# Performance work log

Hardware: AMD Instinct MI355X
Metric: run time of the kernel (lower is better)

## Reference

```python
import jax, jax.numpy as jnp
import numpy as np

B, L, H, E = 8, 4096, 8, 64
NEIGH = 128          # neigh_size: local window length (entries per row of band mask)
SPLITS = 32          # number of Q blocks
L1 = L // SPLITS     # rows per block = 128 (neigh_size <= L/splits holds with equality)


def setup_inputs() -> dict:
    key = jax.random.key(0)
    kq, kk, kv = jax.random.split(key, 3)
    return {
        "queries": jax.random.normal(kq, (B, L, H, E), jnp.float32),
        "keys":    jax.random.normal(kk, (B, L, H, E), jnp.float32),
        "values":  jax.random.normal(kv, (B, L, H, E), jnp.float32),
    }


def reference(queries, keys, values):
    scale = 1.0 / np.sqrt(E)
    # Global key index of each entry in a KV block: block j covers [j*l1 - neigh, j*l1 + l1)
    kv_idx = (jnp.arange(SPLITS)[:, None] * L1
              + jnp.arange(L1 + NEIGH)[None, :] - NEIGH)      # [splits, l1+neigh]
    kv_gather = jnp.clip(kv_idx, 0, L - 1)                    # out-of-range entries get masked

    Qb = queries.reshape(B, SPLITS, L1, H, E)                 # [B, j, l, H, E]
    Kb = keys[:, kv_gather]                                   # [B, j, m, H, E]
    Vb = values[:, kv_gather]                                 # [B, j, m, H, E]

    scores = jnp.einsum('bjlhe,bjmhe->bhjlm', Qb, Kb) * scale # [B, H, splits, l1, l1+neigh]

    # Band: key global index k satisfies q - neigh < k <= q  <=>  l < m <= l + neigh
    l_idx = jnp.arange(L1)[:, None]
    m_idx = jnp.arange(L1 + NEIGH)[None, :]
    band = (m_idx > l_idx) & (m_idx <= l_idx + NEIGH)         # [l1, l1+neigh]
    valid = band[None, :, :] & (kv_idx[:, None, :] >= 0)      # [splits, l1, l1+neigh]

    scores = jnp.where(valid[None, None], scores, jnp.float32(-1e9))
    attn = jax.nn.softmax(scores, axis=-1)
    out = jnp.einsum('bhjlm,bjmhe->bjlhe', attn, Vb)          # [B, splits, l1, H, E]
    return out.reshape(B, L, H, E)
```

## Files before the change

kernel.cpp:

```cpp
#include <hip/hip_runtime.h>

#define B_ 8
#define L_ 4096
#define H_ 8
#define E_ 64
#define NEIGH_ 128
#define SPLITS_ 32
#define BQ 128
#define WIN 256
#define QPAD 72
#define VPAD 264

typedef float f32x4 __attribute__((ext_vector_type(4)));
typedef __bf16 bf16x8 __attribute__((ext_vector_type(8)));
typedef unsigned short u16x4 __attribute__((ext_vector_type(4)));
typedef unsigned short u16x8 __attribute__((ext_vector_type(8)));

__device__ inline unsigned short f2bf(float f) {
  unsigned int u = __float_as_uint(f);
  u += 0x7fff + ((u >> 16) & 1);
  return (unsigned short)(u >> 16);
}

__global__ __launch_bounds__(512) void la_kernel(
    const float* __restrict__ Q, const float* __restrict__ K,
    const float* __restrict__ V, float* __restrict__ out) {
  const int j = blockIdx.x, h = blockIdx.y, b = blockIdx.z;
  const int t = threadIdx.x;

  __shared__ unsigned short Qs[BQ * QPAD];
  __shared__ unsigned short Ks[WIN * QPAD];
  __shared__ unsigned short VsT[E_ * VPAD];
  __shared__ unsigned short Ps[BQ * VPAD];

  const int q0 = j * BQ;
  const int g0 = q0 - NEIGH_;

  for (int i = 0; i < 4; ++i) {
    int idx = t + i * 512;
    int row = idx >> 4, c4 = idx & 15;
    const float4 v = *(const float4*)(Q + ((((size_t)b * L_) + q0 + row) * H_ + h) * E_ + c4 * 4);
    u16x4 p = { f2bf(v.x), f2bf(v.y), f2bf(v.z), f2bf(v.w) };
    *(u16x4*)&Qs[row * QPAD + c4 * 4] = p;
  }
  for (int i = 0; i < 8; ++i) {
    int idx = t + i * 512;
    int km = idx >> 4, c4 = idx & 15;
    int g = g0 + km; g = g < 0 ? 0 : g;
    const float4 v = *(const float4*)(K + ((((size_t)b * L_) + g) * H_ + h) * E_ + c4 * 4);
    u16x4 p = { f2bf(v.x), f2bf(v.y), f2bf(v.z), f2bf(v.w) };
    *(u16x4*)&Ks[km * QPAD + c4 * 4] = p;
  }
  for (int i = 0; i < 8; ++i) {
    int idx = t + i * 512;
    int km = idx >> 4, c4 = idx & 15;
    int g = g0 + km; g = g < 0 ? 0 : g;
    const float4 v = *(const float4*)(V + ((((size_t)b * L_) + g) * H_ + h) * E_ + c4 * 4);
    VsT[(c4 * 4 + 0) * VPAD + km] = f2bf(v.x);
    VsT[(c4 * 4 + 1) * VPAD + km] = f2bf(v.y);
    VsT[(c4 * 4 + 2) * VPAD + km] = f2bf(v.z);
    VsT[(c4 * 4 + 3) * VPAD + km] = f2bf(v.w);
  }
  __syncthreads();

  const int wv = t >> 6, lane = t & 63;
  const int l15 = lane & 15, quad = lane >> 4;
  const int r0 = wv * 16;

  f32x4 S[16];
  for (int kt = 0; kt < 16; ++kt) S[kt] = (f32x4){0.f, 0.f, 0.f, 0.f};
  for (int ks = 0; ks < 2; ++ks) {
    bf16x8 a = __builtin_bit_cast(bf16x8,
        *(const u16x8*)&Qs[(r0 + l15) * QPAD + ks * 32 + quad * 8]);
    for (int kt = 0; kt < 16; ++kt) {
      bf16x8 bb = __builtin_bit_cast(bf16x8,
          *(const u16x8*)&Ks[(kt * 16 + l15) * QPAD + ks * 32 + quad * 8]);
      S[kt] = __builtin_amdgcn_mfma_f32_16x16x32_bf16(a, bb, S[kt], 0, 0, 0);
    }
  }

  float mrow[4] = {-1e30f, -1e30f, -1e30f, -1e30f};
  for (int kt = 0; kt < 16; ++kt) {
    int key = kt * 16 + l15;
    for (int r = 0; r < 4; ++r) {
      int lq = r0 + quad * 4 + r;
      float s = S[kt][r] * 0.125f;
      bool valid = (key > lq) & (key <= lq + NEIGH_) & (g0 + key >= 0);
      s = valid ? s : -1e30f;
      S[kt][r] = s;
      mrow[r] = fmaxf(mrow[r], s);
    }
  }
#pragma unroll
  for (int m = 1; m <= 8; m <<= 1)
    for (int r = 0; r < 4; ++r)
      mrow[r] = fmaxf(mrow[r], __shfl_xor(mrow[r], m));

  float lrow[4] = {0.f, 0.f, 0.f, 0.f};
  for (int kt = 0; kt < 16; ++kt) {
    int key = kt * 16 + l15;
    for (int r = 0; r < 4; ++r) {
      float p = __expf(S[kt][r] - mrow[r]);
      lrow[r] += p;
      Ps[(r0 + quad * 4 + r) * VPAD + key] = f2bf(p);
    }
  }
#pragma unroll
  for (int m = 1; m <= 8; m <<= 1)
    for (int r = 0; r < 4; ++r)
      lrow[r] += __shfl_xor(lrow[r], m);
  float inv[4];
  for (int r = 0; r < 4; ++r) inv[r] = 1.0f / lrow[r];

  __syncthreads();

  f32x4 O[4];
  for (int et = 0; et < 4; ++et) O[et] = (f32x4){0.f, 0.f, 0.f, 0.f};
  for (int ks = 0; ks < 8; ++ks) {
    bf16x8 a = __builtin_bit_cast(bf16x8,
        *(const u16x8*)&Ps[(r0 + l15) * VPAD + ks * 32 + quad * 8]);
    for (int et = 0; et < 4; ++et) {
      bf16x8 bb = __builtin_bit_cast(bf16x8,
          *(const u16x8*)&VsT[(et * 16 + l15) * VPAD + ks * 32 + quad * 8]);
      O[et] = __builtin_amdgcn_mfma_f32_16x16x32_bf16(a, bb, O[et], 0, 0, 0);
    }
  }

  for (int et = 0; et < 4; ++et)
    for (int r = 0; r < 4; ++r) {
      int row = r0 + quad * 4 + r;
      int e = et * 16 + l15;
      out[((((size_t)b * L_) + q0 + row) * H_ + h) * E_ + e] = O[et][r] * inv[r];
    }
}

extern "C" void kernel_launch(void* const* d_in, const int* in_sizes, int n_in,
                              void* d_out, int out_size, void* d_ws, size_t ws_size,
                              hipStream_t stream) {
  const float* q = (const float*)d_in[0];
  const float* k = (const float*)d_in[1];
  const float* v = (const float*)d_in[2];
  float* o = (float*)d_out;
  dim3 grid(SPLITS_, H_, B_);
  la_kernel<<<grid, 512, 0, stream>>>(q, k, v, o);
}
```

Measured before the change: 248.8 us.

## Keep Q and P in registers, swizzle V in LDS, shrink shared memory

Q is loaded straight from global memory into MFMA register fragments, and QK^T is computed transposed (K as the A operand), so each lane owns one query row. The softmax probabilities stay in registers and are redistributed with cross-lane shuffles instead of going through an LDS buffer. V is stored transposed as packed bf16 pairs with an XOR swizzle to avoid bank conflicts. Together with launch_bounds(512,4), the smaller LDS footprint is meant to raise occupancy and cut LDS traffic and one barrier, at the cost of extra shuffle instructions and register pressure.

```diff
diff --git a/kernel.cpp b/kernel.cpp
--- a/kernel.cpp
+++ b/kernel.cpp
@@ -8,129 +8,162 @@
 #define SPLITS_ 32
 #define BQ 128
 #define WIN 256
-#define QPAD 72
-#define VPAD 264
+#define KPAD 72
 
 typedef float f32x4 __attribute__((ext_vector_type(4)));
 typedef __bf16 bf16x8 __attribute__((ext_vector_type(8)));
 typedef unsigned short u16x4 __attribute__((ext_vector_type(4)));
 typedef unsigned short u16x8 __attribute__((ext_vector_type(8)));
+typedef unsigned int u32;
 
 __device__ inline unsigned short f2bf(float f) {
   unsigned int u = __float_as_uint(f);
   u += 0x7fff + ((u >> 16) & 1);
   return (unsigned short)(u >> 16);
 }
+__device__ inline u32 pack2(float a, float b) {
+  return (u32)f2bf(a) | ((u32)f2bf(b) << 16);
+}
 
-__global__ __launch_bounds__(512) void la_kernel(
+__global__ __launch_bounds__(512, 4) void la_kernel(
     const float* __restrict__ Q, const float* __restrict__ K,
     const float* __restrict__ V, float* __restrict__ out) {
   const int j = blockIdx.x, h = blockIdx.y, b = blockIdx.z;
   const int t = threadIdx.x;
 
-  __shared__ unsigned short Qs[BQ * QPAD];
-  __shared__ unsigned short Ks[WIN * QPAD];
-  __shared__ unsigned short VsT[E_ * VPAD];
-  __shared__ unsigned short Ps[BQ * VPAD];
+  __shared__ unsigned short Ks[WIN * KPAD];
+  __shared__ u32 Vs32[E_ * (WIN / 2)];
 
   const int q0 = j * BQ;
   const int g0 = q0 - NEIGH_;
 
-  for (int i = 0; i < 4; ++i) {
-    int idx = t + i * 512;
-    int row = idx >> 4, c4 = idx & 15;
-    const float4 v = *(const float4*)(Q + ((((size_t)b * L_) + q0 + row) * H_ + h) * E_ + c4 * 4);
-    u16x4 p = { f2bf(v.x), f2bf(v.y), f2bf(v.z), f2bf(v.w) };
-    *(u16x4*)&Qs[row * QPAD + c4 * 4] = p;
-  }
   for (int i = 0; i < 8; ++i) {
     int idx = t + i * 512;
     int km = idx >> 4, c4 = idx & 15;
     int g = g0 + km; g = g < 0 ? 0 : g;
     const float4 v = *(const float4*)(K + ((((size_t)b * L_) + g) * H_ + h) * E_ + c4 * 4);
     u16x4 p = { f2bf(v.x), f2bf(v.y), f2bf(v.z), f2bf(v.w) };
-    *(u16x4*)&Ks[km * QPAD + c4 * 4] = p;
+    *(u16x4*)&Ks[km * KPAD + c4 * 4] = p;
   }
-  for (int i = 0; i < 8; ++i) {
+  for (int i = 0; i < 4; ++i) {
     int idx = t + i * 512;
-    int km = idx >> 4, c4 = idx & 15;
-    int g = g0 + km; g = g < 0 ? 0 : g;
-    const float4 v = *(const float4*)(V + ((((size_t)b * L_) + g) * H_ + h) * E_ + c4 * 4);
-    VsT[(c4 * 4 + 0) * VPAD + km] = f2bf(v.x);
-    VsT[(c4 * 4 + 1) * VPAD + km] = f2bf(v.y);
-    VsT[(c4 * 4 + 2) * VPAD + km] = f2bf(v.z);
-    VsT[(c4 * 4 + 3) * VPAD + km] = f2bf(v.w);
+    int kp = idx >> 4, c4 = idx & 15;
+    int k0g = g0 + 2 * kp, k1g = k0g + 1;
+    k0g = k0g < 0 ? 0 : k0g; k1g = k1g < 0 ? 0 : k1g;
+    const float4 v0 = *(const float4*)(V + ((((size_t)b * L_) + k0g) * H_ + h) * E_ + c4 * 4);
+    const float4 v1 = *(const float4*)(V + ((((size_t)b * L_) + k1g) * H_ + h) * E_ + c4 * 4);
+    int g = kp >> 2;
+    int ko = kp & 3;
+    const float a0[4] = {v0.x, v0.y, v0.z, v0.w};
+    const float a1[4] = {v1.x, v1.y, v1.z, v1.w};
+#pragma unroll
+    for (int w = 0; w < 4; ++w) {
+      int e = c4 * 4 + w;
+      int gs = g ^ (e & 31);
+      Vs32[e * 128 + gs * 4 + ko] = pack2(a0[w], a1[w]);
+    }
   }
-  __syncthreads();
 
   const int wv = t >> 6, lane = t & 63;
   const int l15 = lane & 15, quad = lane >> 4;
   const int r0 = wv * 16;
+  const int lq = r0 + l15;
+
+  bf16x8 qfrag[2];
+  {
+    const float* qrow = Q + ((((size_t)b * L_) + q0 + lq) * H_ + h) * E_;
+#pragma unroll
+    for (int ks = 0; ks < 2; ++ks) {
+      const float4 x = *(const float4*)(qrow + ks * 32 + quad * 8);
+      const float4 y = *(const float4*)(qrow + ks * 32 + quad * 8 + 4);
+      u16x8 p = { f2bf(x.x), f2bf(x.y), f2bf(x.z), f2bf(x.w),
+                  f2bf(y.x), f2bf(y.y), f2bf(y.z), f2bf(y.w) };
+      qfrag[ks] = __builtin_bit_cast(bf16x8, p);
+    }
+  }
+  __syncthreads();
 
   f32x4 S[16];
+#pragma unroll
   for (int kt = 0; kt < 16; ++kt) S[kt] = (f32x4){0.f, 0.f, 0.f, 0.f};
+#pragma unroll
   for (int ks = 0; ks < 2; ++ks) {
-    bf16x8 a = __builtin_bit_cast(bf16x8,
-        *(const u16x8*)&Qs[(r0 + l15) * QPAD + ks * 32 + quad * 8]);
+#pragma unroll
     for (int kt = 0; kt < 16; ++kt) {
-      bf16x8 bb = __builtin_bit_cast(bf16x8,
-          *(const u16x8*)&Ks[(kt * 16 + l15) * QPAD + ks * 32 + quad * 8]);
-      S[kt] = __builtin_amdgcn_mfma_f32_16x16x32_bf16(a, bb, S[kt], 0, 0, 0);
+      bf16x8 a = __builtin_bit_cast(bf16x8,
+          *(const u16x8*)&Ks[(kt * 16 + l15) * KPAD + ks * 32 + quad * 8]);
+      S[kt] = __builtin_amdgcn_mfma_f32_16x16x32_bf16(a, qfrag[ks], S[kt], 0, 0, 0);
     }
   }
 
-  float mrow[4] = {-1e30f, -1e30f, -1e30f, -1e30f};
+  float m = -1e30f;
+#pragma unroll
   for (int kt = 0; kt < 16; ++kt) {
-    int key = kt * 16 + l15;
+#pragma unroll
     for (int r = 0; r < 4; ++r) {
-      int lq = r0 + quad * 4 + r;
+      int key = kt * 16 + quad * 4 + r;
       float s = S[kt][r] * 0.125f;
       bool valid = (key > lq) & (key <= lq + NEIGH_) & (g0 + key >= 0);
       s = valid ? s : -1e30f;
       S[kt][r] = s;
-      mrow[r] = fmaxf(mrow[r], s);
+      m = fmaxf(m, s);
     }
   }
+  m = fmaxf(m, __shfl_xor(m, 16));
+  m = fmaxf(m, __shfl_xor(m, 32));
+
+  float lsum = 0.f;
+  u32 pk[16][2];
 #pragma unroll
-  for (int m = 1; m <= 8; m <<= 1)
-    for (int r = 0; r < 4; ++r)
-      mrow[r] = fmaxf(mrow[r], __shfl_xor(mrow[r], m));
-
-  float lrow[4] = {0.f, 0.f, 0.f, 0.f};
   for (int kt = 0; kt < 16; ++kt) {
-    int key = kt * 16 + l15;
-    for (int r = 0; r < 4; ++r) {
-      float p = __expf(S[kt][r] - mrow[r]);
-      lrow[r] += p;
-      Ps[(r0 + quad * 4 + r) * VPAD + key] = f2bf(p);
-    }
+    float p0 = __expf(S[kt][0] - m);
+    float p1 = __expf(S[kt][1] - m);
+    float p2 = __expf(S[kt][2] - m);
+    float p3 = __expf(S[kt][3] - m);
+    lsum += (p0 + p1) + (p2 + p3);
+    pk[kt][0] = pack2(p0, p1);
+    pk[kt][1] = pack2(p2, p3);
   }
-#pragma unroll
-  for (int m = 1; m <= 8; m <<= 1)
-    for (int r = 0; r < 4; ++r)
-      lrow[r] += __shfl_xor(lrow[r], m);
-  float inv[4];
-  for (int r = 0; r < 4; ++r) inv[r] = 1.0f / lrow[r];
-
-  __syncthreads();
+  lsum += __shfl_xor(lsum, 16);
+  lsum += __shfl_xor(lsum, 32);
+  const float inv = 1.0f / lsum;
 
   f32x4 O[4];
+#pragma unroll
   for (int et = 0; et < 4; ++et) O[et] = (f32x4){0.f, 0.f, 0.f, 0.f};
+  const int srcBase = 16 * ((quad & 1) * 2) + l15;
+  const bool hiTile = (quad >> 1) != 0;
+#pragma unroll
   for (int ks = 0; ks < 8; ++ks) {
-    bf16x8 a = __builtin_bit_cast(bf16x8,
-        *(const u16x8*)&Ps[(r0 + l15) * VPAD + ks * 32 + quad * 8]);
+    u32 a32[4];
+#pragma unroll
+    for (int k = 0; k < 4; ++k) {
+      int src = srcBase + 16 * (k >> 1);
+      u32 u0 = (u32)__shfl((int)pk[2 * ks][k & 1], src);
+      u32 u1 = (u32)__shfl((int)pk[2 * ks + 1][k & 1], src);
+      a32[k] = hiTile ? u1 : u0;
+    }
+    bf16x8 afrag = __builtin_bit_cast(bf16x8,
+        (u32 __attribute__((ext_vector_type(4)))){a32[0], a32[1], a32[2], a32[3]});
+#pragma unroll
     for (int et = 0; et < 4; ++et) {
-      bf16x8 bb = __builtin_bit_cast(bf16x8,
-          *(const u16x8*)&VsT[(et * 16 + l15) * VPAD + ks * 32 + quad * 8]);
-      O[et] = __builtin_amdgcn_mfma_f32_16x16x32_bf16(a, bb, O[et], 0, 0, 0);
+      int e = et * 16 + l15;
+      int gs = (ks * 4 + quad) ^ (e & 31);
+      bf16x8 bfrag = __builtin_bit_cast(bf16x8,
+          *(const u16x8*)((const unsigned short*)Vs32 + e * 256 + gs * 8));
+      O[et] = __builtin_amdgcn_mfma_f32_16x16x32_bf16(afrag, bfrag, O[et], 0, 0, 0);
     }
   }
 
+  float invq[4];
+#pragma unroll
+  for (int r = 0; r < 4; ++r) invq[r] = __shfl(inv, quad * 4 + r);
+#pragma unroll
   for (int et = 0; et < 4; ++et)
+#pragma unroll
     for (int r = 0; r < 4; ++r) {
       int row = r0 + quad * 4 + r;
-      int e = et * 16 + l15;
-      out[((((size_t)b * L_) + q0 + row) * H_ + h) * E_ + e] = O[et][r] * inv[r];
+      out[((((size_t)b * L_) + q0 + row) * H_ + h) * E_ + et * 16 + l15] = O[et][r] * invq[r];
     }
 }
 
```

Result: faster. 221.9 us (-10.8%).
